# Kernel tuning notes

Hardware: AMD Instinct MI355X
Metric: run time of the kernel (lower is better)

## Reference

```python
import jax, jax.numpy as jnp
import numpy as np

HEADS = 8
N = 2048; D_IN = 2048; LATENT = 2048; PROJ = 256; HIDDEN = 128
LAGS = 12; E = 65536; EMB = 128; N_ENT = 10000; N_TS = 1000


def _lag_weights(L):
    # weights(): flip(arange(1..L) / (L*(L+1)/2)); sums to 1
    w = np.arange(1, L + 1, dtype=np.float64) / (L * (L + 1) // 2)
    return jnp.asarray(np.ascontiguousarray(w[::-1]), dtype=jnp.float32)


def _gatv2(x, edge_index, Wl, bl, Wr, br, att, bias):
    # GATv2Conv with PyG defaults: self-loops added, leaky_relu(0.2),
    # softmax over incoming edges per target node, concat heads + bias.
    n = x.shape[0]
    H = HEADS
    D = Wl.shape[1] // H
    sl = jnp.arange(n, dtype=edge_index.dtype)
    src = jnp.concatenate([edge_index[0], sl])
    dst = jnp.concatenate([edge_index[1], sl])
    xl = (x @ Wl + bl).reshape(n, H, D)  # source / message transform
    xr = (x @ Wr + br).reshape(n, H, D)  # target transform
    e = jnp.sum(jax.nn.leaky_relu(xl[src] + xr[dst], 0.2) * att, axis=-1)  # [E', H]
    emax = jax.ops.segment_max(e, dst, num_segments=n)
    ee = jnp.exp(e - emax[dst])
    alpha = ee / jax.ops.segment_sum(ee, dst, num_segments=n)[dst]
    out = jax.ops.segment_sum(alpha[:, :, None] * xl[src], dst, num_segments=n)  # [n,H,D]
    return out.reshape(n, H * D) + bias


def _mha(query, lagged, Wq, bq, Wk, bk, Wv, bv):
    # MultiHeadCausalAttention: per-lag K/V projections combined with fixed
    # triangular weights. Since the weights sum to 1, the projection bias
    # passes through the weighted sum unchanged, so the per-lag Python loop
    # fuses into a single einsum over the lag axis.
    n = query.shape[0]
    dim_out = Wq.shape[1]
    dh = dim_out // HEADS
    Q = (query @ Wq + bq).reshape(n, -1, HEADS, dh).transpose(0, 2, 1, 3)  # [n,H,q,dh]
    tw = _lag_weights(lagged.shape[1])
    K = (jnp.einsum('nli,io,l->no', lagged, Wk, tw) + bk).reshape(n, 1, HEADS, dh).transpose(0, 2, 1, 3)
    V = (jnp.einsum('nli,io,l->no', lagged, Wv, tw) + bv).reshape(n, 1, HEADS, dh).transpose(0, 2, 1, 3)
    scores = jnp.einsum('nhqd,nhkd->nhqk', Q, K) / (dh ** 0.5)
    attn = jax.nn.softmax(scores, axis=-1)
    return jnp.einsum('nhqk,nhkd->nhqd', attn, V).transpose(0, 2, 1, 3).reshape(n, -1, dim_out)


def _forward(time_series_data, lagged_data, eps, gumbel_noise,
             entity_table, timestamp_table,
             gat_e_Wl, gat_e_bl, gat_e_Wr, gat_e_br, gat_e_att, gat_e_bias,
             enc_proj_W, enc_proj_b,
             enc_Wq, enc_bq, enc_Wk, enc_bk, enc_Wv, enc_bv,
             enc_fc_W, enc_fc_b,
             dec_Wq, dec_bq, dec_Wk, dec_bk, dec_Wv, dec_bv,
             gat_d_Wl, gat_d_bl, gat_d_Wr, gat_d_br, gat_d_att, gat_d_bias,
             dec_fc_W, dec_fc_b, A_direct, A_indirect,
             entity_indices, timestamp_indices, edge_index):
    entity_emb = entity_table[entity_indices]      # pretrained TKG entity embedding
    ts_emb = timestamp_table[timestamp_indices]    # pretrained TKG timestamp embedding
    feats = jnp.concatenate([time_series_data, entity_emb, ts_emb], axis=-1)
    x = jax.nn.relu(_gatv2(feats, edge_index, gat_e_Wl, gat_e_bl, gat_e_Wr, gat_e_br, gat_e_att, gat_e_bias))
    x = jax.nn.relu(x @ enc_proj_W + enc_proj_b)
    x = jax.nn.relu(_mha(x, lagged_data, enc_Wq, enc_bq, enc_Wk, enc_bk, enc_Wv, enc_bv))  # [N,1,PROJ]
    q_params = x @ enc_fc_W + enc_fc_b
    mean, log_var = jnp.split(q_params, 2, axis=-1)
    z = mean + jnp.exp(0.5 * log_var) * eps  # reparameterization, [N,1,LATENT]
    x = jax.nn.relu(_mha(z, lagged_data, dec_Wq, dec_bq, dec_Wk, dec_bk, dec_Wv, dec_bv))[:, 0, :]
    x = jax.nn.relu(_gatv2(x, edge_index, gat_d_Wl, gat_d_bl, gat_d_Wr, gat_d_br, gat_d_att, gat_d_bias))
    x_rec = x @ dec_fc_W + dec_fc_b  # [N, D_IN]
    direct = A_direct * jnp.sum(x_rec, axis=0)        # einsum('ij,tj->ij')
    indirect = A_indirect * jnp.sum(z, axis=(0, 1))   # einsum('ij,tlj->ij')
    causal_effect = direct + indirect
    y = jax.nn.softmax((causal_effect + gumbel_noise) / 0.5, axis=-1)  # tau=0.5
    hard = jax.nn.one_hot(jnp.argmax(y, axis=-1), y.shape[-1], dtype=y.dtype)
    adj = jax.lax.stop_gradient(hard - y) + y  # hard gumbel-softmax, straight-through
    return z, mean, log_var, x_rec, causal_effect, adj


def setup_inputs():
    key = jax.random.key(0)
    ks = iter(jax.random.split(key, 64))
    def nrm(shape, s=0.02):
        return jax.random.normal(next(ks), shape, jnp.float32) * s
    A0 = jnp.ones((N, N), jnp.float32) + jnp.eye(N, dtype=jnp.float32)
    A0 = A0 / jnp.sum(A0, axis=1)  # matches torch broadcast A0 / A0.sum(1)
    HH = HEADS * HIDDEN
    d = {
        'entity_indices': jax.random.randint(next(ks), (N,), 0, N_ENT),
        'relation_indices': jax.random.randint(next(ks), (N,), 0, N_TS),
        'timestamp_indices': jax.random.randint(next(ks), (N,), 0, N_TS),
        'time_series_data': jax.random.normal(next(ks), (N, D_IN), jnp.float32),
        'edge_index': jax.random.randint(next(ks), (2, E), 0, N),
        'lagged_data': jax.random.normal(next(ks), (N, LAGS, D_IN), jnp.float32),
        'eps': jax.random.normal(next(ks), (N, 1, LATENT), jnp.float32),
        'gumbel_noise': jax.random.gumbel(next(ks), (N, N), jnp.float32),
        'entity_table': nrm((N_ENT, EMB), 1.0),
        'timestamp_table': nrm((N_TS, EMB), 1.0),
        'gat_e_Wl': nrm((D_IN + 2 * EMB, HH)), 'gat_e_bl': jnp.zeros((HH,), jnp.float32),
        'gat_e_Wr': nrm((D_IN + 2 * EMB, HH)), 'gat_e_br': jnp.zeros((HH,), jnp.float32),
        'gat_e_att': nrm((HEADS, HIDDEN), 0.1), 'gat_e_bias': jnp.zeros((HH,), jnp.float32),
        'enc_proj_W': nrm((HH, PROJ)), 'enc_proj_b': jnp.zeros((PROJ,), jnp.float32),
        'enc_Wq': nrm((PROJ, PROJ)), 'enc_bq': jnp.zeros((PROJ,), jnp.float32),
        'enc_Wk': nrm((D_IN, PROJ)), 'enc_bk': jnp.zeros((PROJ,), jnp.float32),
        'enc_Wv': nrm((D_IN, PROJ)), 'enc_bv': jnp.zeros((PROJ,), jnp.float32),
        'enc_fc_W': nrm((PROJ, 2 * LATENT)), 'enc_fc_b': jnp.zeros((2 * LATENT,), jnp.float32),
        'dec_Wq': nrm((LATENT, PROJ)), 'dec_bq': jnp.zeros((PROJ,), jnp.float32),
        'dec_Wk': nrm((D_IN, PROJ)), 'dec_bk': jnp.zeros((PROJ,), jnp.float32),
        'dec_Wv': nrm((D_IN, PROJ)), 'dec_bv': jnp.zeros((PROJ,), jnp.float32),
        'gat_d_Wl': nrm((PROJ, HH)), 'gat_d_bl': jnp.zeros((HH,), jnp.float32),
        'gat_d_Wr': nrm((PROJ, HH)), 'gat_d_br': jnp.zeros((HH,), jnp.float32),
        'gat_d_att': nrm((HEADS, HIDDEN), 0.1), 'gat_d_bias': jnp.zeros((HH,), jnp.float32),
        'dec_fc_W': nrm((HH, D_IN)), 'dec_fc_b': jnp.zeros((D_IN,), jnp.float32),
        'A_direct': A0, 'A_indirect': A0,
    }
    return d


def reference(entity_indices, relation_indices, timestamp_indices, time_series_data,
              edge_index, lagged_data, eps, gumbel_noise,
              entity_table, timestamp_table,
              gat_e_Wl, gat_e_bl, gat_e_Wr, gat_e_br, gat_e_att, gat_e_bias,
              enc_proj_W, enc_proj_b,
              enc_Wq, enc_bq, enc_Wk, enc_bk, enc_Wv, enc_bv,
              enc_fc_W, enc_fc_b,
              dec_Wq, dec_bq, dec_Wk, dec_bk, dec_Wv, dec_bv,
              gat_d_Wl, gat_d_bl, gat_d_Wr, gat_d_br, gat_d_att, gat_d_bias,
              dec_fc_W, dec_fc_b, A_direct, A_indirect):
    # relation_indices are looked up by the pretrained TKG, but the relation
    # embedding is unused downstream in the original forward, so it is ignored.
    return _forward(time_series_data, lagged_data, eps, gumbel_noise,
                    entity_table, timestamp_table,
                    gat_e_Wl, gat_e_bl, gat_e_Wr, gat_e_br, gat_e_att, gat_e_bias,
                    enc_proj_W, enc_proj_b,
                    enc_Wq, enc_bq, enc_Wk, enc_bk, enc_Wv, enc_bv,
                    enc_fc_W, enc_fc_b,
                    dec_Wq, dec_bq, dec_Wk, dec_bk, dec_Wv, dec_bv,
                    gat_d_Wl, gat_d_bl, gat_d_Wr, gat_d_br, gat_d_att, gat_d_bias,
                    dec_fc_W, dec_fc_b, A_direct, A_indirect,
                    entity_indices, timestamp_indices, edge_index)
```

## Files before the change

### kernel.cpp

```cpp
#include <hip/hip_runtime.h>
#include <hip/hip_bf16.h>
#include <math.h>

#define N_NODES 2048
#define DIN     2048
#define HH      1024
#define LAGS    12
#define NE      65536
#define NL      (2048 * 2048)
#define CHUNK   128

#define BM 128
#define BN 128
#define BK 32

typedef __attribute__((ext_vector_type(8))) short short8;
typedef __attribute__((ext_vector_type(4))) float f32x4;

static __device__ __forceinline__ short f2bf_rne(float x) {
  union { float f; unsigned u; } c; c.f = x;
  unsigned u = c.u;
  unsigned r = (u + 0x7fffu + ((u >> 16) & 1u)) >> 16;
  return (short)r;
}
static __device__ __forceinline__ float bf2f(short h) {
  union { unsigned u; float f; } c; c.u = ((unsigned)(unsigned short)h) << 16;
  return c.f;
}

typedef __attribute__((address_space(3))) unsigned int as3_u32;
typedef const __attribute__((address_space(1))) unsigned int as1_u32c;
static __device__ __forceinline__ void gload_lds16(const void* g, void* l) {
  __builtin_amdgcn_global_load_lds((as1_u32c*)g, (as3_u32*)l, 16, 0, 0);
}

#define VMCNT6  asm volatile("s_waitcnt vmcnt(6)" ::: "memory")
#define VMCNT4  asm volatile("s_waitcnt vmcnt(4)" ::: "memory")
#define VMCNT0  asm volatile("s_waitcnt vmcnt(0)" ::: "memory")
#define SBAR()  do { asm volatile("" ::: "memory"); __builtin_amdgcn_s_barrier(); \
                     asm volatile("" ::: "memory"); } while (0)

struct WCfg { const float* W; short* H; short* L; int K; int N; int nb; };
struct WCfg2 { WCfg c[2]; };
struct WCfg4 { WCfg c[4]; };

static __device__ __forceinline__ void wsplit_tile(
    const WCfg& cf, int local, int tid, float t[32][33])
{
  const float* W = cf.W;
  short* H = cf.H;
  short* L = cf.L;
  int K = cf.K, N = cf.N;
  int nbx = N >> 5;
  int bx = local % nbx, by = local / nbx;
  int tx = tid & 31, ty = tid >> 5;
  int c0 = bx << 5, k0 = by << 5;
#pragma unroll
  for (int j = 0; j < 4; ++j)
    t[ty + 8 * j][tx] = W[(size_t)(k0 + ty + 8 * j) * N + c0 + tx];
  __syncthreads();
#pragma unroll
  for (int j = 0; j < 4; ++j) {
    int c = ty + 8 * j;
    float x = t[tx][c];
    short h = f2bf_rne(x);
    size_t off = (size_t)(c0 + c) * K + k0 + tx;
    H[off] = h;
    if (L) L[off] = f2bf_rne(x - bf2f(h));
  }
}

__global__ void init_kernel(int* __restrict__ cursor, float* __restrict__ csx,
                            float* __restrict__ csz) {
  int i = blockIdx.x * 256 + threadIdx.x;
  cursor[i] = 0; csx[i] = 0.f; csz[i] = 0.f;
}

__global__ __launch_bounds__(256) void megaA_kernel(
    const float* __restrict__ lagged, short* __restrict__ lw, WCfg2 cfgs)
{
  __shared__ float t[32][33];
  int bid = blockIdx.x;
  int tid = threadIdx.x;

  if (bid < 2048) {
    int idx = bid * 256 + tid;
    int n = idx >> 8, c8 = idx & 255;
    const float* base = lagged + (size_t)n * (LAGS * DIN) + (size_t)c8 * 8;
    float a[8] = {};
#pragma unroll
    for (int l = 0; l < LAGS; ++l) {
      float w = (float)((double)(LAGS - l) / 78.0);
      float4 v0 = *(const float4*)(base + (size_t)l * DIN);
      float4 v1 = *(const float4*)(base + (size_t)l * DIN + 4);
      a[0] += w * v0.x; a[1] += w * v0.y; a[2] += w * v0.z; a[3] += w * v0.w;
      a[4] += w * v1.x; a[5] += w * v1.y; a[6] += w * v1.z; a[7] += w * v1.w;
    }
    short8 h;
#pragma unroll
    for (int j = 0; j < 8; ++j) h[j] = f2bf_rne(a[j]);
    *(short8*)(lw + (size_t)idx * 8) = h;
  } else {
    int wb = bid - 2048;
    int i = (wb >= cfgs.c[0].nb) ? 1 : 0;
    int local = wb - (i ? cfgs.c[0].nb : 0);
    wsplit_tile(cfgs.c[i], local, tid, t);
  }
}

__global__ __launch_bounds__(256) void megaC_kernel(
    const short* __restrict__ A, const short* __restrict__ Bh0,
    const short* __restrict__ Bh1, short* __restrict__ Cpart,
    WCfg4 cfgs,
    const int* __restrict__ esrc, const int* __restrict__ edst,
    int* __restrict__ cursor, int* __restrict__ csr)
{
  __shared__ char smem[32768];
  int fb = blockIdx.x;
  int tid = threadIdx.x;

  if (fb < 512) {
    short* lds = (short*)smem;
    const int K = 2048, N = 256, M = 2048, klen = 256;
    int lane = tid & 63, wid = tid >> 6;
    int bn = (fb & 1) * BN;
    int bm = ((fb >> 1) & 15) * BM;
    int z = fb >> 5;
    int twin = z & 1;
    int kb = (z >> 1) * klen;
    const short* Bh = twin ? Bh1 : Bh0;

    const short* gp[4];
    int lofs[4];
    {
      int r4 = lane >> 2;
      int ksw = (lane & 3) ^ ((lane >> 3) & 3);
#pragma unroll
      for (int c = 0; c < 4; ++c) {
        int chunk = wid * 4 + c;
        int p = chunk >> 3, s = chunk & 7;
        int r = (s << 4) + r4;
        const short* bp = (p == 0) ? (A + (size_t)(bm + r) * K)
                                   : (Bh + (size_t)(bn + r) * K);
        gp[c] = bp + kb + (ksw << 3);
        lofs[c] = (p << 12) + (s << 9);
      }
    }
    auto stage = [&](int bo) {
#pragma unroll
      for (int c = 0; c < 4; ++c) {
        gload_lds16(gp[c], lds + bo + lofs[c]);
        gp[c] += BK;
      }
    };

    int l15 = lane & 15, l4 = lane >> 4;
    int wr = wid >> 1, wc = wid & 1;
    int soff = (l4 ^ ((l15 >> 1) & 3)) << 3;
    int aoff[4], bhoff[4];
#pragma unroll
    for (int i = 0; i < 4; ++i) {
      int r = wr * 64 + i * 16 + l15;
      int c = wc * 64 + i * 16 + l15;
      aoff[i]  = r * BK + soff;
      bhoff[i] = 4096 + c * BK + soff;
    }

    f32x4 acc[4][4];
#pragma unroll
    for (int m = 0; m < 4; ++m)
#pragma unroll
      for (int n = 0; n < 4; ++n) acc[m][n] = (f32x4){0.f, 0.f, 0.f, 0.f};

    stage(0);
    int cur = 0;
#pragma unroll
    for (int t = 0; t < 8; ++t) {
      if (t + 1 < 8) { stage(cur ? 0 : 8192); VMCNT4; }
      else { VMCNT0; }
      SBAR();
      const short* rb = lds + (cur ? 8192 : 0);
      short8 af[4], bh8[4];
#pragma unroll
      for (int i = 0; i < 4; ++i) {
        af[i]  = *(const short8*)(rb + aoff[i]);
        bh8[i] = *(const short8*)(rb + bhoff[i]);
      }
#pragma unroll
      for (int m = 0; m < 4; ++m)
#pragma unroll
        for (int n = 0; n < 4; ++n)
          acc[m][n] = __builtin_amdgcn_mfma_f32_16x16x32_bf16(af[m], bh8[n], acc[m][n], 0, 0, 0);
      SBAR();
      cur ^= 1;
    }

    short* P = Cpart + (size_t)z * ((size_t)M * N);
#pragma unroll
    for (int n = 0; n < 4; ++n) {
      int col = bn + wc * 64 + n * 16 + l15;
#pragma unroll
      for (int m = 0; m < 4; ++m) {
        int row0 = bm + wr * 64 + m * 16 + (l4 << 2);
#pragma unroll
        for (int r = 0; r < 4; ++r)
          P[(size_t)(row0 + r) * N + col] = f2bf_rne(acc[m][n][r]);
      }
    }
  } else if (fb < 4096) {
    float (*t)[33] = (float(*)[33])smem;
    int wb = fb - 512;
    int i = 0, base = 0;
    while (i < 3 && wb >= base + cfgs.c[i].nb) { base += cfgs.c[i].nb; ++i; }
    wsplit_tile(cfgs.c[i], wb - base, tid, t);
  } else {
    int i = (fb - 4096) * 256 + tid;
    if (i < NE) {
      int d = edst[i];
      int p = atomicAdd(&cursor[d], 1);
      if (p < 128) csr[(d << 7) + p] = esrc[i];
    } else if (i < NE + N_NODES) {
      int nn = i - NE;
      int p = atomicAdd(&cursor[nn], 1);
      if (p < 128) csr[(nn << 7) + p] = nn;
    }
  }
}

__global__ __launch_bounds__(256) void gemm_p3(
    const short* __restrict__ A,
    const short* __restrict__ Bh0, const short* __restrict__ Bl0,
    const short* __restrict__ Bh1, const short* __restrict__ Bl1,
    short* __restrict__ Cpart,
    int M, int N, int K, int klen, int ntwin)
{
  __shared__ short lds[2 * 12288];
  int tid = threadIdx.x;
  int lane = tid & 63, wid = tid >> 6;
  int bn = blockIdx.x * BN, bm = blockIdx.y * BM;
  int z = blockIdx.z;
  int twin = (ntwin == 2) ? (z & 1) : 0;
  int kchunk = (ntwin == 2) ? (z >> 1) : z;
  int kb = kchunk * klen;
  const short* Bh = twin ? Bh1 : Bh0;
  const short* Bl = twin ? Bl1 : Bl0;

  const short* gp[6];
  int lofs[6];
  {
    int r4 = lane >> 2;
    int ksw = (lane & 3) ^ ((lane >> 3) & 3);
#pragma unroll
    for (int c = 0; c < 6; ++c) {
      int chunk = wid * 6 + c;
      int p = chunk >> 3, s = chunk & 7;
      int r = (s << 4) + r4;
      const short* bp = (p == 0) ? (A + (size_t)(bm + r) * K)
                      : (p == 1) ? (Bh + (size_t)(bn + r) * K)
                                 : (Bl + (size_t)(bn + r) * K);
      gp[c] = bp + kb + (ksw << 3);
      lofs[c] = (p << 12) + (s << 9);
    }
  }
  auto stage = [&](int bo) {
#pragma unroll
    for (int c = 0; c < 6; ++c) {
      gload_lds16(gp[c], lds + bo + lofs[c]);
      gp[c] += BK;
    }
  };

  int l15 = lane & 15, l4 = lane >> 4;
  int wr = wid >> 1, wc = wid & 1;
  int soff = (l4 ^ ((l15 >> 1) & 3)) << 3;
  int aoff[4], bhoff[4], bloff[4];
#pragma unroll
  for (int i = 0; i < 4; ++i) {
    int r = wr * 64 + i * 16 + l15;
    int c = wc * 64 + i * 16 + l15;
    aoff[i]  = r * BK + soff;
    bhoff[i] = 4096 + c * BK + soff;
    bloff[i] = 8192 + c * BK + soff;
  }

  f32x4 acc[4][4];
#pragma unroll
  for (int m = 0; m < 4; ++m)
#pragma unroll
    for (int n = 0; n < 4; ++n) acc[m][n] = (f32x4){0.f, 0.f, 0.f, 0.f};

  int nt = klen / BK;
  stage(0);
  int cur = 0;
  for (int t = 0; t < nt; ++t) {
    if (t + 1 < nt) { stage(cur ? 0 : 12288); VMCNT6; }
    else { VMCNT0; }
    SBAR();
    const short* rb = lds + (cur ? 12288 : 0);
    short8 af[4], bh8[4], bl8[4];
#pragma unroll
    for (int i = 0; i < 4; ++i) {
      af[i]  = *(const short8*)(rb + aoff[i]);
      bh8[i] = *(const short8*)(rb + bhoff[i]);
      bl8[i] = *(const short8*)(rb + bloff[i]);
    }
#pragma unroll
    for (int m = 0; m < 4; ++m)
#pragma unroll
      for (int n = 0; n < 4; ++n) {
        acc[m][n] = __builtin_amdgcn_mfma_f32_16x16x32_bf16(af[m], bh8[n], acc[m][n], 0, 0, 0);
        acc[m][n] = __builtin_amdgcn_mfma_f32_16x16x32_bf16(af[m], bl8[n], acc[m][n], 0, 0, 0);
      }
    SBAR();
    cur ^= 1;
  }

  short* P = Cpart + (size_t)z * ((size_t)M * N);
#pragma unroll
  for (int n = 0; n < 4; ++n) {
    int col = bn + wc * 64 + n * 16 + l15;
#pragma unroll
    for (int m = 0; m < 4; ++m) {
      int row0 = bm + wr * 64 + m * 16 + (l4 << 2);
#pragma unroll
      for (int r = 0; r < 4; ++r)
        P[(size_t)(row0 + r) * N + col] = f2bf_rne(acc[m][n][r]);
    }
  }
}

__global__ __launch_bounds__(256) void gemm_dual(
    const short* __restrict__ xe, const short* __restrict__ xd,
    const short* __restrict__ fcH, const short* __restrict__ fcL,
    const short* __restrict__ WlH, const short* __restrict__ WlL,
    const short* __restrict__ WrH, const short* __restrict__ WrL,
    const float* __restrict__ fc_b, const float* __restrict__ bl,
    const float* __restrict__ br,
    float* __restrict__ out_mean, float* __restrict__ out_lv,
    short* __restrict__ xl, short* __restrict__ xr)
{
  __shared__ short lds[2 * 12288];
  const int K = 256;
  int fb = blockIdx.x;
  const short *A, *Bh, *Bl;
  const float* bias;
  int bm, bn, jobB, ldc;
  short* Obf = nullptr;
  float* Of = nullptr;
  if (fb < 512) {
    A = xe; Bh = fcH; Bl = fcL; bias = fc_b;
    bn = (fb & 31) << 7; bm = (fb >> 5) << 7;
    jobB = 0; ldc = 2048; Of = out_mean;
  } else {
    int g = fb - 512, twin = g & 1, t = g >> 1;
    A = xd; Bh = twin ? WrH : WlH; Bl = twin ? WrL : WlL;
    bias = twin ? br : bl;
    bn = (t & 7) << 7; bm = (t >> 3) << 7;
    jobB = 1; ldc = 1024; Obf = twin ? xr : xl;
  }

  int tid = threadIdx.x;
  int lane = tid & 63, wid = tid >> 6;

  const short* gp[6];
  int lofs[6];
  {
    int r4 = lane >> 2;
    int ksw = (lane & 3) ^ ((lane >> 3) & 3);
#pragma unroll
    for (int c = 0; c < 6; ++c) {
      int chunk = wid * 6 + c;
      int p = chunk >> 3, s = chunk & 7;
      int r = (s << 4) + r4;
      const short* bp = (p == 0) ? (A + (size_t)(bm + r) * K)
                      : (p == 1) ? (Bh + (size_t)(bn + r) * K)
                                 : (Bl + (size_t)(bn + r) * K);
      gp[c] = bp + (ksw << 3);
      lofs[c] = (p << 12) + (s << 9);
    }
  }
  auto stage = [&](int bo) {
#pragma unroll
    for (int c = 0; c < 6; ++c) {
      gload_lds16(gp[c], lds + bo + lofs[c]);
      gp[c] += BK;
    }
  };

  int l15 = lane & 15, l4 = lane >> 4;
  int wr = wid >> 1, wc = wid & 1;
  int soff = (l4 ^ ((l15 >> 1) & 3)) << 3;
  int aoff[4], bhoff[4], bloff[4];
#pragma unroll
  for (int i = 0; i < 4; ++i) {
    int r = wr * 64 + i * 16 + l15;
    int c = wc * 64 + i * 16 + l15;
    aoff[i]  = r * BK + soff;
    bhoff[i] = 4096 + c * BK + soff;
    bloff[i] = 8192 + c * BK + soff;
  }

  f32x4 acc[4][4];
#pragma unroll
  for (int m = 0; m < 4; ++m)
#pragma unroll
    for (int n = 0; n < 4; ++n) acc[m][n] = (f32x4){0.f, 0.f, 0.f, 0.f};

  stage(0);
  int cur = 0;
#pragma unroll
  for (int t = 0; t < 8; ++t) {
    if (t + 1 < 8) { stage(cur ? 0 : 12288); VMCNT6; }
    else { VMCNT0; }
    SBAR();
    const short* rb = lds + (cur ? 12288 : 0);
    short8 af[4], bh8[4], bl8[4];
#pragma unroll
    for (int i = 0; i < 4; ++i) {
      af[i]  = *(const short8*)(rb + aoff[i]);
      bh8[i] = *(const short8*)(rb + bhoff[i]);
      bl8[i] = *(const short8*)(rb + bloff[i]);
    }
#pragma unroll
    for (int m = 0; m < 4; ++m)
#pragma unroll
      for (int n = 0; n < 4; ++n) {
        acc[m][n] = __builtin_amdgcn_mfma_f32_16x16x32_bf16(af[m], bh8[n], acc[m][n], 0, 0, 0);
        acc[m][n] = __builtin_amdgcn_mfma_f32_16x16x32_bf16(af[m], bl8[n], acc[m][n], 0, 0, 0);
      }
    SBAR();
    cur ^= 1;
  }

#pragma unroll
  for (int n = 0; n < 4; ++n) {
    int col = bn + wc * 64 + n * 16 + l15;
    float bv = bias[col];
    if (jobB) {
#pragma unroll
      for (int m = 0; m < 4; ++m) {
        int row0 = bm + wr * 64 + m * 16 + (l4 << 2);
#pragma unroll
        for (int r = 0; r < 4; ++r)
          Obf[(size_t)(row0 + r) * ldc + col] = f2bf_rne(acc[m][n][r] + bv);
      }
    } else {
      float* O = Of; int oc = col;
      if (col >= 2048) { O = out_lv; oc = col - 2048; }
#pragma unroll
      for (int m = 0; m < 4; ++m) {
        int row0 = bm + wr * 64 + m * 16 + (l4 << 2);
#pragma unroll
        for (int r = 0; r < 4; ++r)
          O[(size_t)(row0 + r) * ldc + oc] = acc[m][n][r] + bv;
      }
    }
  }
}

__global__ __launch_bounds__(256) void sumrelu_kernel(
    const short* __restrict__ part, const float* __restrict__ b0,
    const float* __restrict__ b1, short* __restrict__ xe,
    short* __restrict__ xd)
{
  int i4 = blockIdx.x * 256 + threadIdx.x;
  size_t S = (size_t)N_NODES * 256;
  size_t base = (size_t)i4 * 4;
  int col = (int)(base & 255);
  float4 b0v = *(const float4*)(b0 + col);
  float4 b1v = *(const float4*)(b1 + col);
  float s0[4] = {}, s1[4] = {};
#pragma unroll
  for (int c = 0; c < 8; ++c) {
    short4 p0 = *(const short4*)(part + (size_t)(2 * c) * S + base);
    short4 p1 = *(const short4*)(part + (size_t)(2 * c + 1) * S + base);
    s0[0] += bf2f(p0.x); s0[1] += bf2f(p0.y); s0[2] += bf2f(p0.z); s0[3] += bf2f(p0.w);
    s1[0] += bf2f(p1.x); s1[1] += bf2f(p1.y); s1[2] += bf2f(p1.z); s1[3] += bf2f(p1.w);
  }
  short4 e, d;
  e.x = f2bf_rne(fmaxf(s0[0] + b0v.x, 0.f));
  e.y = f2bf_rne(fmaxf(s0[1] + b0v.y, 0.f));
  e.z = f2bf_rne(fmaxf(s0[2] + b0v.z, 0.f));
  e.w = f2bf_rne(fmaxf(s0[3] + b0v.w, 0.f));
  d.x = f2bf_rne(fmaxf(s1[0] + b1v.x, 0.f));
  d.y = f2bf_rne(fmaxf(s1[1] + b1v.y, 0.f));
  d.z = f2bf_rne(fmaxf(s1[2] + b1v.z, 0.f));
  d.w = f2bf_rne(fmaxf(s1[3] + b1v.w, 0.f));
  *(short4*)(xe + base) = e;
  *(short4*)(xd + base) = d;
}

__global__ __launch_bounds__(256) void megaB_kernel(
    const short* __restrict__ xl, const short* __restrict__ xr,
    const float* __restrict__ att, const float* __restrict__ bias,
    const int* __restrict__ csr, const int* __restrict__ cursor,
    short* __restrict__ outp,
    const float* __restrict__ mean_in, const float* __restrict__ lv_in,
    const float* __restrict__ eps, float* __restrict__ z,
    float* __restrict__ csz)
{
  __shared__ float xr_s[HH];
  __shared__ float att_s[HH];
  __shared__ float e_s[8 * CHUNK];
  __shared__ int   src_s[CHUNK];
  __shared__ float m_s[8], s_s[8], f_s[8];

  int tid = threadIdx.x;

  if (blockIdx.x >= 2048) {
    int flat = blockIdx.x - 2048;
    int c = ((flat & 3) * 256 + tid) * 2;
    int r0 = (flat >> 2) * 16;
    float sx = 0.f, sy = 0.f;
    for (int r = r0; r < r0 + 16; ++r) {
      size_t off = (size_t)r * 2048 + c;
      float2 m = *(const float2*)(mean_in + off);
      float2 v = *(const float2*)(lv_in + off);
      float2 e = *(const float2*)(eps + off);
      float zx = m.x + expf(0.5f * v.x) * e.x;
      float zy = m.y + expf(0.5f * v.y) * e.y;
      *(float2*)(z + off) = make_float2(zx, zy);
      sx += zx; sy += zy;
    }
    atomicAdd(&csz[c], sx);
    atomicAdd(&csz[c + 1], sy);
    return;
  }

  int n = blockIdx.x;
  {
    short4 x4 = ((const short4*)(xr + (size_t)n * HH))[tid];
    xr_s[tid * 4 + 0] = bf2f(x4.x);
    xr_s[tid * 4 + 1] = bf2f(x4.y);
    xr_s[tid * 4 + 2] = bf2f(x4.z);
    xr_s[tid * 4 + 3] = bf2f(x4.w);
  }
  ((float4*)att_s)[tid] = ((const float4*)att)[tid];
  if (tid < 8) { m_s[tid] = -INFINITY; s_s[tid] = 0.f; }
  __syncthreads();

  int beg = n << 7;
  int cnt_total = min(cursor[n], 128);
  int end = beg + cnt_total;
  int ht = tid >> 5;
  float4 acc = make_float4(0.f, 0.f, 0.f, 0.f);

  for (int c0 = beg; c0 < end; c0 += CHUNK) {
    int cnt = min(CHUNK, end - c0);
    if (tid < cnt) src_s[tid] = csr[c0 + tid];
    __syncthreads();

    int wave = tid >> 6, lane = tid & 63;
    int d0 = lane << 4;
    for (int e = wave; e < cnt; e += 4) {
      const short* xlr = xl + (size_t)src_s[e] * HH + d0;
      short8 a0 = *(const short8*)xlr;
      short8 a1 = *(const short8*)(xlr + 8);
      float sum = 0.f;
#pragma unroll
      for (int j = 0; j < 8; ++j) {
        float t = bf2f(a0[j]) + xr_s[d0 + j];
        t = t > 0.f ? t : 0.2f * t;
        sum += t * att_s[d0 + j];
      }
#pragma unroll
      for (int j = 0; j < 8; ++j) {
        float t = bf2f(a1[j]) + xr_s[d0 + 8 + j];
        t = t > 0.f ? t : 0.2f * t;
        sum += t * att_s[d0 + 8 + j];
      }
      sum += __shfl_xor(sum, 1);
      sum += __shfl_xor(sum, 2);
      sum += __shfl_xor(sum, 4);
      if ((lane & 7) == 0) e_s[(lane >> 3) * CHUNK + e] = sum;
    }
    __syncthreads();

    {
      int h = tid >> 5, i0 = tid & 31;
      float cm = -INFINITY;
      for (int e = i0; e < cnt; e += 32) cm = fmaxf(cm, e_s[h * CHUNK + e]);
#pragma unroll
      for (int m = 1; m < 32; m <<= 1) cm = fmaxf(cm, __shfl_xor(cm, m));
      float m_old = m_s[h];
      float m_new = fmaxf(m_old, cm);
      float csum = 0.f;
      for (int e = i0; e < cnt; e += 32) {
        float p = expf(e_s[h * CHUNK + e] - m_new);
        e_s[h * CHUNK + e] = p;
        csum += p;
      }
#pragma unroll
      for (int m = 1; m < 32; m <<= 1) csum += __shfl_xor(csum, m);
      if (i0 == 0) {
        float f = expf(m_old - m_new);
        s_s[h] = s_s[h] * f + csum;
        m_s[h] = m_new;
        f_s[h] = f;
      }
    }
    __syncthreads();

    float f = f_s[ht];
    acc.x *= f; acc.y *= f; acc.z *= f; acc.w *= f;
    for (int e = 0; e < cnt; ++e) {
      float p = e_s[ht * CHUNK + e];
      short4 v = *(const short4*)(xl + (size_t)src_s[e] * HH + (tid << 2));
      acc.x += p * bf2f(v.x); acc.y += p * bf2f(v.y);
      acc.z += p * bf2f(v.z); acc.w += p * bf2f(v.w);
    }
    __syncthreads();
  }

  float inv = 1.0f / s_s[ht];
  float4 b4 = *(const float4*)(bias + (tid << 2));
  short4 o4;
  o4.x = f2bf_rne(fmaxf(acc.x * inv + b4.x, 0.f));
  o4.y = f2bf_rne(fmaxf(acc.y * inv + b4.y, 0.f));
  o4.z = f2bf_rne(fmaxf(acc.z * inv + b4.z, 0.f));
  o4.w = f2bf_rne(fmaxf(acc.w * inv + b4.w, 0.f));
  *(short4*)(outp + (size_t)n * HH + (tid << 2)) = o4;
}

__global__ __launch_bounds__(256) void xrec_sum_kernel(
    const short* __restrict__ part, const float* __restrict__ bias,
    float* __restrict__ xrec, float* __restrict__ csx)
{
  int c = (blockIdx.x * 256 + threadIdx.x) * 2;
  int r0 = blockIdx.y * 16;
  size_t S = (size_t)N_NODES * 2048;
  float2 b = *(const float2*)(bias + c);
  float sx = 0.f, sy = 0.f;
  for (int r = r0; r < r0 + 16; ++r) {
    size_t off = (size_t)r * 2048 + c;
    short2 p0 = *(const short2*)(part + off);
    short2 p1 = *(const short2*)(part + S + off);
    float vx = bf2f(p0.x) + bf2f(p1.x) + b.x;
    float vy = bf2f(p0.y) + bf2f(p1.y) + b.y;
    *(float2*)(xrec + off) = make_float2(vx, vy);
    sx += vx; sy += vy;
  }
  atomicAdd(&csx[c], sx);
  atomicAdd(&csx[c + 1], sy);
}

__global__ __launch_bounds__(256) void final_kernel(
    const float* __restrict__ Ad, const float* __restrict__ Ai,
    const float* __restrict__ gum, const float* __restrict__ csx,
    const float* __restrict__ csz, float* __restrict__ ce_out,
    float* __restrict__ adj_out)
{
  int i = blockIdx.x;
  int tid = threadIdx.x;
  size_t rb = (size_t)i * 2048;

  float vmax = -INFINITY; int vidx = 0;
  for (int j4 = tid; j4 < 512; j4 += 256) {
    float4 ad = *(const float4*)(Ad  + rb + (size_t)j4 * 4);
    float4 ai = *(const float4*)(Ai  + rb + (size_t)j4 * 4);
    float4 g  = *(const float4*)(gum + rb + (size_t)j4 * 4);
    float4 cx = *(const float4*)(csx + (size_t)j4 * 4);
    float4 cz = *(const float4*)(csz + (size_t)j4 * 4);
    float4 ce;
    ce.x = ad.x * cx.x + ai.x * cz.x;
    ce.y = ad.y * cx.y + ai.y * cz.y;
    ce.z = ad.z * cx.z + ai.z * cz.z;
    ce.w = ad.w * cx.w + ai.w * cz.w;
    *(float4*)(ce_out + rb + (size_t)j4 * 4) = ce;
    int j = j4 * 4;
    float l;
    l = (ce.x + g.x) * 2.0f; if (l > vmax) { vmax = l; vidx = j; }
    l = (ce.y + g.y) * 2.0f; if (l > vmax) { vmax = l; vidx = j + 1; }
    l = (ce.z + g.z) * 2.0f; if (l > vmax) { vmax = l; vidx = j + 2; }
    l = (ce.w + g.w) * 2.0f; if (l > vmax) { vmax = l; vidx = j + 3; }
  }
  for (int m = 1; m < 64; m <<= 1) {
    float ov = __shfl_xor(vmax, m);
    int   oi = __shfl_xor(vidx, m);
    if (ov > vmax || (ov == vmax && oi < vidx)) { vmax = ov; vidx = oi; }
  }
  __shared__ float wm[4];
  __shared__ int   wi[4];
  __shared__ int   amax;
  int lane = tid & 63, wave = tid >> 6;
  if (lane == 0) { wm[wave] = vmax; wi[wave] = vidx; }
  __syncthreads();
  if (tid == 0) {
    float bv = wm[0]; int bi = wi[0];
    for (int w = 1; w < 4; ++w)
      if (wm[w] > bv || (wm[w] == bv && wi[w] < bi)) { bv = wm[w]; bi = wi[w]; }
    amax = bi;
  }
  __syncthreads();
  int am = amax;
  for (int j4 = tid; j4 < 512; j4 += 256) {
    int j = j4 * 4;
    float4 o;
    o.x = (j     == am) ? 1.f : 0.f;
    o.y = (j + 1 == am) ? 1.f : 0.f;
    o.z = (j + 2 == am) ? 1.f : 0.f;
    o.w = (j + 3 == am) ? 1.f : 0.f;
    *(float4*)(adj_out + rb + (size_t)j4 * 4) = o;
  }
}

extern "C" void kernel_launch(void* const* d_in, const int* in_sizes, int n_in,
                              void* d_out, int out_size, void* d_ws, size_t ws_size,
                              hipStream_t stream) {
  (void)in_sizes; (void)n_in; (void)out_size; (void)ws_size;

  const int*   edge_index = (const int*)d_in[4];
  const float* lagged     = (const float*)d_in[5];
  const float* eps        = (const float*)d_in[6];
  const float* gumbel     = (const float*)d_in[7];
  const float* enc_Wv     = (const float*)d_in[22];
  const float* enc_bv     = (const float*)d_in[23];
  const float* enc_fc_W   = (const float*)d_in[24];
  const float* enc_fc_b   = (const float*)d_in[25];
  const float* dec_Wv     = (const float*)d_in[30];
  const float* dec_bv     = (const float*)d_in[31];
  const float* gat_Wl     = (const float*)d_in[32];
  const float* gat_bl     = (const float*)d_in[33];
  const float* gat_Wr     = (const float*)d_in[34];
  const float* gat_br     = (const float*)d_in[35];
  const float* gat_att    = (const float*)d_in[36];
  const float* gat_bias   = (const float*)d_in[37];
  const float* dec_fc_W   = (const float*)d_in[38];
  const float* dec_fc_b   = (const float*)d_in[39];
  const float* A_dir      = (const float*)d_in[40];
  const float* A_ind      = (const float*)d_in[41];

  float* out      = (float*)d_out;
  float* out_z    = out;
  float* out_mean = out + (size_t)NL;
  float* out_lv   = out + 2 * (size_t)NL;
  float* out_xrec = out + 3 * (size_t)NL;
  float* out_ce   = out + 4 * (size_t)NL;
  float* out_adj  = out + 5 * (size_t)NL;

  char* ws = (char*)d_ws;
  short* lw_bf = (short*)(ws);
  short* WvH0  = (short*)(ws + ((size_t) 8 << 20));
  short* WvH1  = (short*)(ws + ((size_t)10 << 20));
  short* fcH   = (short*)(ws + ((size_t)12 << 20));
  short* fcL   = (short*)(ws + ((size_t)14 << 20));
  short* WlH   = (short*)(ws + ((size_t)16 << 20));
  short* WlL   = (short*)(ws + ((size_t)16 << 20) + (512u << 10));
  short* WrH   = (short*)(ws + ((size_t)17 << 20));
  short* WrL   = (short*)(ws + ((size_t)17 << 20) + (512u << 10));
  short* dfH   = (short*)(ws + ((size_t)18 << 20));
  short* dfL   = (short*)(ws + ((size_t)22 << 20));
  short* xe_bf = (short*)(ws + ((size_t)26 << 20));
  short* xd_bf = (short*)(ws + ((size_t)27 << 20));
  short* xl    = (short*)(ws + ((size_t)28 << 20));
  short* xr    = (short*)(ws + ((size_t)32 << 20));
  short* gt_bf = (short*)(ws + ((size_t)44 << 20));
  short* part  = (short*)(ws + ((size_t)48 << 20));
  int*   cursor = (int*) (ws + ((size_t)64 << 20));
  int*   csr    = (int*) (ws + ((size_t)64 << 20) + (64u << 10));
  float* csx    = (float*)(ws + ((size_t)66 << 20));
  float* csz    = (float*)(ws + ((size_t)66 << 20) + (16u << 10));

  const int* e_src = edge_index;
  const int* e_dst = edge_index + NE;

  init_kernel<<<8, 256, 0, stream>>>(cursor, csx, csz);

  {
    WCfg2 c2;
    c2.c[0] = { enc_Wv, WvH0, nullptr, 2048, 256, 512 };
    c2.c[1] = { dec_Wv, WvH1, nullptr, 2048, 256, 512 };
    megaA_kernel<<<3072, 256, 0, stream>>>(lagged, lw_bf, c2);
  }

  {
    WCfg4 c4;
    c4.c[0] = { enc_fc_W, fcH, fcL, 256,  4096, 1024 };
    c4.c[1] = { gat_Wl,   WlH, WlL, 256,  1024, 256  };
    c4.c[2] = { gat_Wr,   WrH, WrL, 256,  1024, 256  };
    c4.c[3] = { dec_fc_W, dfH, dfL, 1024, 2048, 2048 };
    megaC_kernel<<<4360, 256, 0, stream>>>(
        lw_bf, WvH0, WvH1, part, c4, e_src, e_dst, cursor, csr);
  }

  sumrelu_kernel<<<512, 256, 0, stream>>>(part, enc_bv, dec_bv, xe_bf, xd_bf);

  gemm_dual<<<768, 256, 0, stream>>>(
      xe_bf, xd_bf, fcH, fcL, WlH, WlL, WrH, WrL,
      enc_fc_b, gat_bl, gat_br, out_mean, out_lv, xl, xr);

  megaB_kernel<<<2560, 256, 0, stream>>>(
      xl, xr, gat_att, gat_bias, csr, cursor, gt_bf,
      out_mean, out_lv, eps, out_z, csz);

  gemm_p3<<<dim3(16, 16, 2), 256, 0, stream>>>(
      gt_bf, dfH, dfL, nullptr, nullptr, part,
      N_NODES, 2048, 1024, 512, 1);
  xrec_sum_kernel<<<dim3(4, 128), 256, 0, stream>>>(part, dec_fc_b, out_xrec, csx);

  final_kernel<<<N_NODES, 256, 0, stream>>>(A_dir, A_ind, gumbel, csx, csz,
                                            out_ce, out_adj);
}
```

Baseline: 195.1 us.

## Drop low-part split from decoder fc GEMM, fold its column-sum correction algebraically

The decoder output GEMM no longer multiplies by the bf16 low-residual weight matrix, which halves its MFMA work and B-tile LDS traffic. To keep the column sums used downstream exact-ish, the GAT output column sums are accumulated with atomics and dotted with the low-part weights in the reduction kernel. The separate init kernel is folded into megaA as extra blocks. The reconstructed output itself now loses the low-part precision contribution, and megaB gains many atomics on a 1024-float buffer.

```diff
diff --git a/kernel.cpp b/kernel.cpp
--- a/kernel.cpp
+++ b/kernel.cpp
@@ -70,14 +70,10 @@
   }
 }
 
-__global__ void init_kernel(int* __restrict__ cursor, float* __restrict__ csx,
-                            float* __restrict__ csz) {
-  int i = blockIdx.x * 256 + threadIdx.x;
-  cursor[i] = 0; csx[i] = 0.f; csz[i] = 0.f;
-}
-
 __global__ __launch_bounds__(256) void megaA_kernel(
-    const float* __restrict__ lagged, short* __restrict__ lw, WCfg2 cfgs)
+    const float* __restrict__ lagged, short* __restrict__ lw, WCfg2 cfgs,
+    int* __restrict__ cursor, float* __restrict__ csx,
+    float* __restrict__ csz, float* __restrict__ cs_gat)
 {
   __shared__ float t[32][33];
   int bid = blockIdx.x;
@@ -100,11 +96,15 @@
 #pragma unroll
     for (int j = 0; j < 8; ++j) h[j] = f2bf_rne(a[j]);
     *(short8*)(lw + (size_t)idx * 8) = h;
-  } else {
+  } else if (bid < 3072) {
     int wb = bid - 2048;
     int i = (wb >= cfgs.c[0].nb) ? 1 : 0;
     int local = wb - (i ? cfgs.c[0].nb : 0);
     wsplit_tile(cfgs.c[i], local, tid, t);
+  } else {
+    int i = (bid - 3072) * 256 + tid;
+    cursor[i] = 0; csx[i] = 0.f; csz[i] = 0.f;
+    if (i < 1024) cs_gat[i] = 0.f;
   }
 }
 
@@ -227,44 +227,37 @@
   }
 }
 
-__global__ __launch_bounds__(256) void gemm_p3(
-    const short* __restrict__ A,
-    const short* __restrict__ Bh0, const short* __restrict__ Bl0,
-    const short* __restrict__ Bh1, const short* __restrict__ Bl1,
-    short* __restrict__ Cpart,
-    int M, int N, int K, int klen, int ntwin)
+__global__ __launch_bounds__(256) void gemm_xrec(
+    const short* __restrict__ A, const short* __restrict__ Bh,
+    short* __restrict__ Cpart)
 {
-  __shared__ short lds[2 * 12288];
+  __shared__ short lds[2 * 8192];
+  const int K = 1024, N = 2048, M = 2048, klen = 512;
   int tid = threadIdx.x;
   int lane = tid & 63, wid = tid >> 6;
   int bn = blockIdx.x * BN, bm = blockIdx.y * BM;
   int z = blockIdx.z;
-  int twin = (ntwin == 2) ? (z & 1) : 0;
-  int kchunk = (ntwin == 2) ? (z >> 1) : z;
-  int kb = kchunk * klen;
-  const short* Bh = twin ? Bh1 : Bh0;
-  const short* Bl = twin ? Bl1 : Bl0;
-
-  const short* gp[6];
-  int lofs[6];
+  int kb = z * klen;
+
+  const short* gp[4];
+  int lofs[4];
   {
     int r4 = lane >> 2;
     int ksw = (lane & 3) ^ ((lane >> 3) & 3);
 #pragma unroll
-    for (int c = 0; c < 6; ++c) {
-      int chunk = wid * 6 + c;
+    for (int c = 0; c < 4; ++c) {
+      int chunk = wid * 4 + c;
       int p = chunk >> 3, s = chunk & 7;
       int r = (s << 4) + r4;
       const short* bp = (p == 0) ? (A + (size_t)(bm + r) * K)
-                      : (p == 1) ? (Bh + (size_t)(bn + r) * K)
-                                 : (Bl + (size_t)(bn + r) * K);
+                                 : (Bh + (size_t)(bn + r) * K);
       gp[c] = bp + kb + (ksw << 3);
       lofs[c] = (p << 12) + (s << 9);
     }
   }
   auto stage = [&](int bo) {
 #pragma unroll
-    for (int c = 0; c < 6; ++c) {
+    for (int c = 0; c < 4; ++c) {
       gload_lds16(gp[c], lds + bo + lofs[c]);
       gp[c] += BK;
     }
@@ -273,14 +266,13 @@
   int l15 = lane & 15, l4 = lane >> 4;
   int wr = wid >> 1, wc = wid & 1;
   int soff = (l4 ^ ((l15 >> 1) & 3)) << 3;
-  int aoff[4], bhoff[4], bloff[4];
+  int aoff[4], bhoff[4];
 #pragma unroll
   for (int i = 0; i < 4; ++i) {
     int r = wr * 64 + i * 16 + l15;
     int c = wc * 64 + i * 16 + l15;
     aoff[i]  = r * BK + soff;
     bhoff[i] = 4096 + c * BK + soff;
-    bloff[i] = 8192 + c * BK + soff;
   }
 
   f32x4 acc[4][4];
@@ -289,28 +281,25 @@
 #pragma unroll
     for (int n = 0; n < 4; ++n) acc[m][n] = (f32x4){0.f, 0.f, 0.f, 0.f};
 
-  int nt = klen / BK;
+  const int nt = klen / BK;
   stage(0);
   int cur = 0;
   for (int t = 0; t < nt; ++t) {
-    if (t + 1 < nt) { stage(cur ? 0 : 12288); VMCNT6; }
+    if (t + 1 < nt) { stage(cur ? 0 : 8192); VMCNT4; }
     else { VMCNT0; }
     SBAR();
-    const short* rb = lds + (cur ? 12288 : 0);
-    short8 af[4], bh8[4], bl8[4];
+    const short* rb = lds + (cur ? 8192 : 0);
+    short8 af[4], bh8[4];
 #pragma unroll
     for (int i = 0; i < 4; ++i) {
       af[i]  = *(const short8*)(rb + aoff[i]);
       bh8[i] = *(const short8*)(rb + bhoff[i]);
-      bl8[i] = *(const short8*)(rb + bloff[i]);
     }
 #pragma unroll
     for (int m = 0; m < 4; ++m)
 #pragma unroll
-      for (int n = 0; n < 4; ++n) {
+      for (int n = 0; n < 4; ++n)
         acc[m][n] = __builtin_amdgcn_mfma_f32_16x16x32_bf16(af[m], bh8[n], acc[m][n], 0, 0, 0);
-        acc[m][n] = __builtin_amdgcn_mfma_f32_16x16x32_bf16(af[m], bl8[n], acc[m][n], 0, 0, 0);
-      }
     SBAR();
     cur ^= 1;
   }
@@ -494,7 +483,7 @@
     const short* __restrict__ xl, const short* __restrict__ xr,
     const float* __restrict__ att, const float* __restrict__ bias,
     const int* __restrict__ csr, const int* __restrict__ cursor,
-    short* __restrict__ outp,
+    short* __restrict__ outp, float* __restrict__ cs_gat,
     const float* __restrict__ mean_in, const float* __restrict__ lv_in,
     const float* __restrict__ eps, float* __restrict__ z,
     float* __restrict__ csz)
@@ -620,11 +609,16 @@
   o4.z = f2bf_rne(fmaxf(acc.z * inv + b4.z, 0.f));
   o4.w = f2bf_rne(fmaxf(acc.w * inv + b4.w, 0.f));
   *(short4*)(outp + (size_t)n * HH + (tid << 2)) = o4;
+  atomicAdd(&cs_gat[tid * 4 + 0], bf2f(o4.x));
+  atomicAdd(&cs_gat[tid * 4 + 1], bf2f(o4.y));
+  atomicAdd(&cs_gat[tid * 4 + 2], bf2f(o4.z));
+  atomicAdd(&cs_gat[tid * 4 + 3], bf2f(o4.w));
 }
 
 __global__ __launch_bounds__(256) void xrec_sum_kernel(
     const short* __restrict__ part, const float* __restrict__ bias,
-    float* __restrict__ xrec, float* __restrict__ csx)
+    float* __restrict__ xrec, float* __restrict__ csx,
+    const float* __restrict__ cs_gat, const short* __restrict__ dfL)
 {
   int c = (blockIdx.x * 256 + threadIdx.x) * 2;
   int r0 = blockIdx.y * 16;
@@ -639,6 +633,19 @@
     float vy = bf2f(p0.y) + bf2f(p1.y) + b.y;
     *(float2*)(xrec + off) = make_float2(vx, vy);
     sx += vx; sy += vy;
+  }
+  if (blockIdx.y == 0) {
+    const short* rw0 = dfL + (size_t)c * 1024;
+    const short* rw1 = dfL + (size_t)(c + 1) * 1024;
+    float a0 = 0.f, a1 = 0.f;
+    for (int k = 0; k < 1024; k += 4) {
+      float4 g = *(const float4*)(cs_gat + k);
+      short4 w0 = *(const short4*)(rw0 + k);
+      short4 w1 = *(const short4*)(rw1 + k);
+      a0 += g.x * bf2f(w0.x) + g.y * bf2f(w0.y) + g.z * bf2f(w0.z) + g.w * bf2f(w0.w);
+      a1 += g.x * bf2f(w1.x) + g.y * bf2f(w1.y) + g.z * bf2f(w1.z) + g.w * bf2f(w1.w);
+    }
+    sx += a0; sy += a1;
   }
   atomicAdd(&csx[c], sx);
   atomicAdd(&csx[c + 1], sy);
@@ -760,17 +767,17 @@
   int*   csr    = (int*) (ws + ((size_t)64 << 20) + (64u << 10));
   float* csx    = (float*)(ws + ((size_t)66 << 20));
   float* csz    = (float*)(ws + ((size_t)66 << 20) + (16u << 10));
+  float* cs_gat = (float*)(ws + ((size_t)66 << 20) + (32u << 10));
 
   const int* e_src = edge_index;
   const int* e_dst = edge_index + NE;
-
-  init_kernel<<<8, 256, 0, stream>>>(cursor, csx, csz);
 
   {
     WCfg2 c2;
     c2.c[0] = { enc_Wv, WvH0, nullptr, 2048, 256, 512 };
     c2.c[1] = { dec_Wv, WvH1, nullptr, 2048, 256, 512 };
-    megaA_kernel<<<3072, 256, 0, stream>>>(lagged, lw_bf, c2);
+    megaA_kernel<<<3080, 256, 0, stream>>>(lagged, lw_bf, c2,
+                                           cursor, csx, csz, cs_gat);
   }
 
   {
@@ -790,13 +797,12 @@
       enc_fc_b, gat_bl, gat_br, out_mean, out_lv, xl, xr);
 
   megaB_kernel<<<2560, 256, 0, stream>>>(
-      xl, xr, gat_att, gat_bias, csr, cursor, gt_bf,
+      xl, xr, gat_att, gat_bias, csr, cursor, gt_bf, cs_gat,
       out_mean, out_lv, eps, out_z, csz);
 
-  gemm_p3<<<dim3(16, 16, 2), 256, 0, stream>>>(
-      gt_bf, dfH, dfL, nullptr, nullptr, part,
-      N_NODES, 2048, 1024, 512, 1);
-  xrec_sum_kernel<<<dim3(4, 128), 256, 0, stream>>>(part, dec_fc_b, out_xrec, csx);
+  gemm_xrec<<<dim3(16, 16, 2), 256, 0, stream>>>(gt_bf, dfH, part);
+  xrec_sum_kernel<<<dim3(4, 128), 256, 0, stream>>>(
+      part, dec_fc_b, out_xrec, csx, cs_gat, dfL);
 
   final_kernel<<<N_NODES, 256, 0, stream>>>(A_dir, A_ind, gumbel, csx, csz,
                                             out_ce, out_adj);
```

Result: slower. 385.1 us (+97.4%).
